# Optimization experiments

Measured on AMD Instinct MI355X. Metric: run time of the kernel, lower is better.

## Reference

```python
import jax, jax.numpy as jnp
import numpy as np

N = 2000
E = 128
H = 8
DH = E // H
K = 32  # max_neighbors
CLAMP = 1e4


def _sanitize(t):
    t = jnp.nan_to_num(t, nan=0.0, posinf=CLAMP, neginf=-CLAMP)
    return jnp.clip(t, -CLAMP, CLAMP)


def _layernorm(h, g, b, eps=1e-5):
    mu = h.mean(-1, keepdims=True)
    var = ((h - mu) ** 2).mean(-1, keepdims=True)
    return (h - mu) * jax.lax.rsqrt(var + eps) * g + b


def setup_inputs() -> dict:
    key = jax.random.key(0)
    ks = jax.random.split(key, 8)
    x = jax.random.normal(ks[0], (N, E), dtype=jnp.float32)
    coords9 = jax.random.normal(ks[1], (N, 9), dtype=jnp.float32)
    prompt_signal = jax.random.normal(ks[2], (E,), dtype=jnp.float32)
    pe_w = jax.random.normal(ks[3], (3, 32), dtype=jnp.float32) / np.sqrt(3.0)
    pe_b = jnp.zeros((32,), jnp.float32)
    pe_g = jnp.ones((32,), jnp.float32)
    pe_bt = jnp.zeros((32,), jnp.float32)
    in_w = jax.random.normal(ks[4], (3 * E, E), dtype=jnp.float32) / np.sqrt(E)
    in_b = jnp.zeros((3 * E,), jnp.float32)
    out_w = jax.random.normal(ks[5], (E, E), dtype=jnp.float32) / np.sqrt(E)
    out_b = jnp.zeros((E,), jnp.float32)
    return {"x": x, "coords9": coords9, "prompt_signal": prompt_signal,
            "pe_w": pe_w, "pe_b": pe_b, "pe_g": pe_g, "pe_bt": pe_bt,
            "in_w": in_w, "in_b": in_b, "out_w": out_w, "out_b": out_b}


def reference(x, coords9, prompt_signal, pe_w, pe_b, pe_g, pe_bt, in_w, in_b, out_w, out_b):
    n = x.shape[0]
    verts = coords9.reshape(n, 3, 3)
    cent = verts.mean(axis=1)  # (N,3)

    # pairwise centroid distances (only geo-relation channel that affects the output;
    # cos_angles/area_ratios/boundary_sharing feed geo_bias which is dead code in forward)
    diff = cent[:, None, :] - cent[None, :, :]
    dist = jnp.sqrt(jnp.sum(diff * diff, axis=-1) + 1e-20)  # (N,N)

    # positional encoder: Linear(3,32) -> GELU(exact) -> LayerNorm(32)
    pe = jax.nn.gelu(cent @ pe_w + pe_b, approximate=False)
    pe = _layernorm(pe, pe_g, pe_bt)  # (N,32)

    prompt_enhanced = x + prompt_signal[None, :]
    pos_enhanced = jnp.concatenate([prompt_enhanced[:, : 3 * E // 4], pe], axis=-1)  # (N,128)

    # top-K nearest neighbors -> additive attention mask (0 for kept, -inf-like otherwise)
    _, topk_idx = jax.lax.top_k(-dist, K)  # (N,K) smallest distances
    big_neg = jnp.float32(-1e9)
    attn_mask = jnp.full((n, n), big_neg, dtype=jnp.float32)
    attn_mask = attn_mask.at[jnp.arange(n)[:, None], topk_idx].set(0.0)

    # nn.MultiheadAttention (self-attention, eval mode -> no dropout)
    qkv = pos_enhanced @ in_w.T + in_b  # (N,3E)
    q, k, v = jnp.split(qkv, 3, axis=-1)
    q = q.reshape(n, H, DH).transpose(1, 0, 2)  # (H,N,DH)
    k = k.reshape(n, H, DH).transpose(1, 0, 2)
    v = v.reshape(n, H, DH).transpose(1, 0, 2)
    scores = jnp.einsum('hnd,hmd->hnm', q, k) / np.sqrt(DH) + attn_mask[None]
    probs = jax.nn.softmax(scores, axis=-1)
    o = jnp.einsum('hnm,hmd->hnd', probs, v)  # (H,N,DH)
    o = o.transpose(1, 0, 2).reshape(n, E)
    out = o @ out_w.T + out_b
    return _sanitize(out)
```

## Files before the change

kernel.cpp:

```cpp
#include <hip/hip_runtime.h>
#include <math.h>

#define N_NODES 2000
#define E_DIM   128
#define QKV_W   384
#define LDA     36
#define GEMM_BLOCKS 189

__global__ __launch_bounds__(256) void prep_qkv_kernel(
    const float* __restrict__ x, const float* __restrict__ coords9,
    const float* __restrict__ ps, const float* __restrict__ pe_w,
    const float* __restrict__ pe_b, const float* __restrict__ pe_g,
    const float* __restrict__ pe_bt, const float* __restrict__ in_w,
    const float* __restrict__ in_b, const float* __restrict__ out_w,
    float4* __restrict__ cw, float* __restrict__ qkv,
    float* __restrict__ out_wT)
{
    __shared__ __align__(16) float As[E_DIM * LDA];
    int tid = threadIdx.x;

    if (blockIdx.x >= GEMM_BLOCKS) {
        int bid2 = blockIdx.x - GEMM_BLOCKS;
        int g2 = tid >> 5, lane2 = tid & 31;
        int k = bid2 * 8 + g2;
        #pragma unroll
        for (int m = 0; m < 4; ++m) {
            int e = lane2 + 32 * m;
            out_wT[k * 128 + e] = out_w[e * 128 + k];
        }
        return;
    }

    int rt = blockIdx.x / 3, ct = blockIdx.x % 3;
    int rbase = rt * 32, cbase = ct * 128;
    int g = tid >> 5, lane = tid & 31;

    #pragma unroll
    for (int rr = 0; rr < 4; ++rr) {
        int rl = rr * 8 + g;
        int row = rbase + rl;
        bool vr = (row < N_NODES);
        float cx = 0.f, cy = 0.f, cz = 0.f;
        if (vr) {
            const float* c9 = coords9 + row * 9;
            cx = (c9[0] + c9[3] + c9[6]) * (1.0f / 3.0f);
            cy = (c9[1] + c9[4] + c9[7]) * (1.0f / 3.0f);
            cz = (c9[2] + c9[5] + c9[8]) * (1.0f / 3.0f);
        }
        if (ct == 0 && vr && lane == 0) {
            float4 c4; c4.x = cx; c4.y = cy; c4.z = cz; c4.w = 0.f;
            cw[row] = c4;
        }

        #pragma unroll
        for (int k = 0; k < 3; ++k) {
            int c = lane + 32 * k;
            float v = vr ? (x[row * E_DIM + c] + ps[c]) : 0.f;
            As[c * LDA + rl] = v;
        }

        int j = lane;
        float h = cx * pe_w[j] + cy * pe_w[32 + j] + cz * pe_w[64 + j] + pe_b[j];
        float ge = 0.5f * h * (1.0f + erff(h * 0.7071067811865476f));
        float s = ge;
        #pragma unroll
        for (int m = 16; m >= 1; m >>= 1) s += __shfl_xor(s, m);
        float mu = s * (1.0f / 32.0f);
        float d = ge - mu;
        float v2 = d * d;
        #pragma unroll
        for (int m = 16; m >= 1; m >>= 1) v2 += __shfl_xor(v2, m);
        float var = v2 * (1.0f / 32.0f);
        float y = d * (1.0f / sqrtf(var + 1e-5f)) * pe_g[j] + pe_bt[j];
        As[(96 + j) * LDA + rl] = vr ? y : 0.f;
    }
    __syncthreads();

    int cg = tid & 31, rg = tid >> 5;
    int c0 = cbase + cg * 4, r0 = rg * 4;
    float acc[4][4];
    #pragma unroll
    for (int i = 0; i < 4; ++i)
        #pragma unroll
        for (int jj = 0; jj < 4; ++jj) acc[i][jj] = 0.f;

    for (int k0 = 0; k0 < 128; k0 += 4) {
        float4 a0 = *(const float4*)&As[(k0 + 0) * LDA + r0];
        float4 a1 = *(const float4*)&As[(k0 + 1) * LDA + r0];
        float4 a2 = *(const float4*)&As[(k0 + 2) * LDA + r0];
        float4 a3 = *(const float4*)&As[(k0 + 3) * LDA + r0];
        #pragma unroll
        for (int ci = 0; ci < 4; ++ci) {
            float4 b = *(const float4*)&in_w[(c0 + ci) * E_DIM + k0];
            acc[0][ci] += a0.x * b.x + a1.x * b.y + a2.x * b.z + a3.x * b.w;
            acc[1][ci] += a0.y * b.x + a1.y * b.y + a2.y * b.z + a3.y * b.w;
            acc[2][ci] += a0.z * b.x + a1.z * b.y + a2.z * b.z + a3.z * b.w;
            acc[3][ci] += a0.w * b.x + a1.w * b.y + a2.w * b.z + a3.w * b.w;
        }
    }

    #pragma unroll
    for (int ri = 0; ri < 4; ++ri) {
        int row = rbase + r0 + ri;
        if (row < N_NODES) {
            float4 o4;
            o4.x = acc[ri][0] + in_b[c0 + 0];
            o4.y = acc[ri][1] + in_b[c0 + 1];
            o4.z = acc[ri][2] + in_b[c0 + 2];
            o4.w = acc[ri][3] + in_b[c0 + 3];
            *(float4*)&qkv[row * QKV_W + c0] = o4;
        }
    }
}

__device__ __forceinline__ float sanitize(float v)
{
    v = (v == v) ? v : 0.f;
    return fminf(fmaxf(v, -1e4f), 1e4f);
}

__global__ __launch_bounds__(256) void attn_proj_kernel(
    const float4* __restrict__ cw, const float* __restrict__ qkv,
    const float* __restrict__ out_wT, const float* __restrict__ out_b,
    float* __restrict__ out)
{
    __shared__ unsigned int hist[512];
    __shared__ float wMin[4], wMax[4];
    __shared__ int sh_b, sh_nless, sh_sel, sh_eq;
    __shared__ int waveSum[4];
    __shared__ int topk[32];
    __shared__ int eqIdx[256];
    __shared__ unsigned int eqKey[256];
    __shared__ __align__(16) float qs[128];
    __shared__ float pr[256];
    __shared__ __align__(16) float os[128];

    int tid = threadIdx.x;
    int row = blockIdx.x;
    int lane = tid & 63, wid = tid >> 6;

    float4 ci = cw[row];
    float cix = ci.x, ciy = ci.y, ciz = ci.z;
    unsigned int kbits[8];
    int bins[8];
    bool valid[8];
    float lmin = __int_as_float(0x7f800000);
    float lmax = __int_as_float(0xff800000);
    {
        #pragma clang fp contract(off)
        #pragma unroll
        for (int l = 0; l < 8; ++l) {
            int j = tid + 256 * l;
            valid[l] = (j < N_NODES);
            float key = __int_as_float(0x7f800000);
            if (valid[l]) {
                float4 cj = cw[j];
                float dx = cix - cj.x;
                float dy = ciy - cj.y;
                float dz = ciz - cj.z;
                float a = dx * dx;
                float b = dy * dy;
                float c = dz * dz;
                float d2 = ((a + b) + c) + 1e-20f;
                key = sqrtf(d2);
                lmin = fminf(lmin, key);
                lmax = fmaxf(lmax, key);
            }
            kbits[l] = __float_as_uint(key);
        }
    }

    #pragma unroll
    for (int m = 32; m >= 1; m >>= 1) {
        lmin = fminf(lmin, __shfl_xor(lmin, m));
        lmax = fmaxf(lmax, __shfl_xor(lmax, m));
    }
    if (lane == 0) { wMin[wid] = lmin; wMax[wid] = lmax; }
    hist[tid] = 0u;
    hist[tid + 256] = 0u;
    if (tid == 0) { sh_sel = 0; sh_eq = 0; }
    __syncthreads();
    float lo = fminf(fminf(wMin[0], wMin[1]), fminf(wMin[2], wMin[3]));
    float hi = fmaxf(fmaxf(wMax[0], wMax[1]), fmaxf(wMax[2], wMax[3]));
    float scale = 255.0f / fmaxf(hi - lo, 1e-30f);

    unsigned int hsel = (wid & 1) << 8;
    #pragma unroll
    for (int l = 0; l < 8; ++l) {
        int bin = 255;
        if (valid[l]) {
            float key = __uint_as_float(kbits[l]);
            bin = (int)((key - lo) * scale);
            bin = min(max(bin, 0), 255);
            atomicAdd(&hist[hsel + bin], 1u);
        }
        bins[l] = bin;
    }
    __syncthreads();

    int h = (int)(hist[tid] + hist[tid + 256]);
    int incl = h;
    #pragma unroll
    for (int dd = 1; dd < 64; dd <<= 1) {
        int u = __shfl_up(incl, dd);
        if (lane >= dd) incl += u;
    }
    if (lane == 63) waveSum[wid] = incl;
    __syncthreads();
    int off = 0;
    for (int w = 0; w < wid; ++w) off += waveSum[w];
    int cum = incl + off;
    if (cum >= 32 && (cum - h) < 32) {
        sh_b = tid;
        sh_nless = cum - h;
    }
    __syncthreads();

    int b = sh_b;
    int req = 32 - sh_nless;

    #pragma unroll
    for (int l = 0; l < 8; ++l) {
        if (valid[l]) {
            int bin = bins[l];
            int j = tid + 256 * l;
            if (bin < b) {
                int p = atomicAdd(&sh_sel, 1);
                topk[p] = j;
            } else if (bin == b) {
                int e = atomicAdd(&sh_eq, 1);
                if (e < 256) { eqIdx[e] = j; eqKey[e] = kbits[l]; }
            }
        }
    }
    if (tid < 128) qs[tid] = qkv[row * QKV_W + tid];
    __syncthreads();

    int eq = min(sh_eq, 256);
    if (tid < eq) {
        int myIdx = eqIdx[tid];
        unsigned int myKey = eqKey[tid];
        int rank = 0;
        for (int u = 0; u < eq; ++u) {
            unsigned int ku = eqKey[u];
            rank += (ku < myKey || (ku == myKey && eqIdx[u] < myIdx)) ? 1 : 0;
        }
        if (rank < req) {
            int p = atomicAdd(&sh_sel, 1);
            topk[p] = myIdx;
        }
    }
    __syncthreads();

    {
        int hh = tid >> 5, j = tid & 31;
        int jj = topk[j];
        const float4* kp = (const float4*)&qkv[jj * QKV_W + 128 + hh * 16];
        const float4* qp = (const float4*)&qs[hh * 16];
        float s = 0.f;
        #pragma unroll
        for (int i = 0; i < 4; ++i) {
            float4 kv = kp[i], qv = qp[i];
            s += qv.x * kv.x + qv.y * kv.y + qv.z * kv.z + qv.w * kv.w;
        }
        s *= 0.25f;
        float m = s;
        #pragma unroll
        for (int msk = 16; msk >= 1; msk >>= 1) m = fmaxf(m, __shfl_xor(m, msk));
        float p = expf(s - m);
        float su = p;
        #pragma unroll
        for (int msk = 16; msk >= 1; msk >>= 1) su += __shfl_xor(su, msk);
        pr[tid] = p / su;
    }
    __syncthreads();

    if (tid < 128) {
        int hh = tid >> 4;
        float acc = 0.f;
        #pragma unroll
        for (int j = 0; j < 32; ++j) {
            int jj = topk[j];
            acc += pr[hh * 32 + j] * qkv[jj * QKV_W + 256 + tid];
        }
        os[tid] = acc;
    }
    __syncthreads();

    if (tid < 128) {
        float a = 0.f;
        #pragma unroll
        for (int k = 0; k < 128; k += 4) {
            a += os[k + 0] * out_wT[(k + 0) * 128 + tid]
               + os[k + 1] * out_wT[(k + 1) * 128 + tid]
               + os[k + 2] * out_wT[(k + 2) * 128 + tid]
               + os[k + 3] * out_wT[(k + 3) * 128 + tid];
        }
        out[row * E_DIM + tid] = sanitize(a + out_b[tid]);
    }
}

extern "C" void kernel_launch(void* const* d_in, const int* in_sizes, int n_in,
                              void* d_out, int out_size, void* d_ws, size_t ws_size,
                              hipStream_t stream)
{
    const float* x      = (const float*)d_in[0];
    const float* coords = (const float*)d_in[1];
    const float* ps     = (const float*)d_in[2];
    const float* pe_w   = (const float*)d_in[3];
    const float* pe_b   = (const float*)d_in[4];
    const float* pe_g   = (const float*)d_in[5];
    const float* pe_bt  = (const float*)d_in[6];
    const float* in_w   = (const float*)d_in[7];
    const float* in_b   = (const float*)d_in[8];
    const float* out_w  = (const float*)d_in[9];
    const float* out_b  = (const float*)d_in[10];
    float* out = (float*)d_out;

    float* ws    = (float*)d_ws;
    float4* cw   = (float4*)ws;
    float* qkvb  = ws + 8192;
    float* owT   = ws + 8192 + 768000;

    prep_qkv_kernel<<<GEMM_BLOCKS + 16, 256, 0, stream>>>(
        x, coords, ps, pe_w, pe_b, pe_g, pe_bt, in_w, in_b, out_w,
        cw, qkvb, owT);
    attn_proj_kernel<<<2000, 256, 0, stream>>>(cw, qkvb, owT, out_b, out);
}
```

Measured before the change: 113.4 us.

## Process two query rows per block in attention kernel

Each block of the attention/projection kernel now handles two rows instead of one, launching half as many blocks. The candidate centroid loads are shared between both rows' distance computations, and the previously idle half of the threads now work in the value aggregation and output projection stages. This doubles shared memory and register use per block, which may reduce occupancy and serializes some per-row stages such as the tie-ranking and softmax.

```diff
diff --git a/kernel.cpp b/kernel.cpp
--- a/kernel.cpp
+++ b/kernel.cpp
@@ -124,143 +124,181 @@
     const float* __restrict__ out_wT, const float* __restrict__ out_b,
     float* __restrict__ out)
 {
-    __shared__ unsigned int hist[512];
-    __shared__ float wMin[4], wMax[4];
-    __shared__ int sh_b, sh_nless, sh_sel, sh_eq;
-    __shared__ int waveSum[4];
-    __shared__ int topk[32];
-    __shared__ int eqIdx[256];
-    __shared__ unsigned int eqKey[256];
-    __shared__ __align__(16) float qs[128];
-    __shared__ float pr[256];
-    __shared__ __align__(16) float os[128];
+    __shared__ unsigned int hist[1024];
+    __shared__ float wMinA[4], wMaxA[4], wMinB[4], wMaxB[4];
+    __shared__ int sh_b[2], sh_nless[2], sh_sel[2], sh_eq[2];
+    __shared__ int waveSumA[4], waveSumB[4];
+    __shared__ int topkA[32], topkB[32];
+    __shared__ int eqIdxA[256], eqIdxB[256];
+    __shared__ unsigned int eqKeyA[256], eqKeyB[256];
+    __shared__ __align__(16) float qsA[128], qsB[128];
+    __shared__ float prA[256], prB[256];
+    __shared__ __align__(16) float osA[128], osB[128];
 
     int tid = threadIdx.x;
-    int row = blockIdx.x;
+    int rA = blockIdx.x * 2, rB = rA + 1;
     int lane = tid & 63, wid = tid >> 6;
 
-    float4 ci = cw[row];
-    float cix = ci.x, ciy = ci.y, ciz = ci.z;
-    unsigned int kbits[8];
-    int bins[8];
+    float4 cAv = cw[rA], cBv = cw[rB];
+    unsigned int kbA[8], kbB[8];
+    int binsA[8], binsB[8];
     bool valid[8];
-    float lmin = __int_as_float(0x7f800000);
-    float lmax = __int_as_float(0xff800000);
+    float lminA = __int_as_float(0x7f800000), lmaxA = __int_as_float(0xff800000);
+    float lminB = __int_as_float(0x7f800000), lmaxB = __int_as_float(0xff800000);
     {
         #pragma clang fp contract(off)
         #pragma unroll
         for (int l = 0; l < 8; ++l) {
             int j = tid + 256 * l;
             valid[l] = (j < N_NODES);
-            float key = __int_as_float(0x7f800000);
+            float keyA = __int_as_float(0x7f800000);
+            float keyB = __int_as_float(0x7f800000);
             if (valid[l]) {
                 float4 cj = cw[j];
-                float dx = cix - cj.x;
-                float dy = ciy - cj.y;
-                float dz = ciz - cj.z;
-                float a = dx * dx;
-                float b = dy * dy;
-                float c = dz * dz;
-                float d2 = ((a + b) + c) + 1e-20f;
-                key = sqrtf(d2);
-                lmin = fminf(lmin, key);
-                lmax = fmaxf(lmax, key);
+                float dxA = cAv.x - cj.x, dyA = cAv.y - cj.y, dzA = cAv.z - cj.z;
+                float aA = dxA * dxA, bA = dyA * dyA, cA_ = dzA * dzA;
+                float d2A = ((aA + bA) + cA_) + 1e-20f;
+                keyA = sqrtf(d2A);
+                lminA = fminf(lminA, keyA);
+                lmaxA = fmaxf(lmaxA, keyA);
+                float dxB = cBv.x - cj.x, dyB = cBv.y - cj.y, dzB = cBv.z - cj.z;
+                float aB = dxB * dxB, bB = dyB * dyB, cB_ = dzB * dzB;
+                float d2B = ((aB + bB) + cB_) + 1e-20f;
+                keyB = sqrtf(d2B);
+                lminB = fminf(lminB, keyB);
+                lmaxB = fmaxf(lmaxB, keyB);
             }
-            kbits[l] = __float_as_uint(key);
+            kbA[l] = __float_as_uint(keyA);
+            kbB[l] = __float_as_uint(keyB);
         }
     }
 
     #pragma unroll
     for (int m = 32; m >= 1; m >>= 1) {
-        lmin = fminf(lmin, __shfl_xor(lmin, m));
-        lmax = fmaxf(lmax, __shfl_xor(lmax, m));
-    }
-    if (lane == 0) { wMin[wid] = lmin; wMax[wid] = lmax; }
-    hist[tid] = 0u;
-    hist[tid + 256] = 0u;
-    if (tid == 0) { sh_sel = 0; sh_eq = 0; }
-    __syncthreads();
-    float lo = fminf(fminf(wMin[0], wMin[1]), fminf(wMin[2], wMin[3]));
-    float hi = fmaxf(fmaxf(wMax[0], wMax[1]), fmaxf(wMax[2], wMax[3]));
-    float scale = 255.0f / fmaxf(hi - lo, 1e-30f);
-
-    unsigned int hsel = (wid & 1) << 8;
+        lminA = fminf(lminA, __shfl_xor(lminA, m));
+        lmaxA = fmaxf(lmaxA, __shfl_xor(lmaxA, m));
+        lminB = fminf(lminB, __shfl_xor(lminB, m));
+        lmaxB = fmaxf(lmaxB, __shfl_xor(lmaxB, m));
+    }
+    if (lane == 0) {
+        wMinA[wid] = lminA; wMaxA[wid] = lmaxA;
+        wMinB[wid] = lminB; wMaxB[wid] = lmaxB;
+    }
+    hist[tid] = 0u; hist[tid + 256] = 0u; hist[tid + 512] = 0u; hist[tid + 768] = 0u;
+    if (tid == 0) { sh_sel[0] = 0; sh_sel[1] = 0; sh_eq[0] = 0; sh_eq[1] = 0; }
+    __syncthreads();
+    float loA = fminf(fminf(wMinA[0], wMinA[1]), fminf(wMinA[2], wMinA[3]));
+    float hiA = fmaxf(fmaxf(wMaxA[0], wMaxA[1]), fmaxf(wMaxA[2], wMaxA[3]));
+    float scaleA = 255.0f / fmaxf(hiA - loA, 1e-30f);
+    float loB = fminf(fminf(wMinB[0], wMinB[1]), fminf(wMinB[2], wMinB[3]));
+    float hiB = fmaxf(fmaxf(wMaxB[0], wMaxB[1]), fmaxf(wMaxB[2], wMaxB[3]));
+    float scaleB = 255.0f / fmaxf(hiB - loB, 1e-30f);
+
+    unsigned int hselA = (unsigned int)(wid & 1) << 8;
+    unsigned int hselB = 512u + ((unsigned int)(wid & 1) << 8);
     #pragma unroll
     for (int l = 0; l < 8; ++l) {
-        int bin = 255;
+        int binA = 255, binB = 255;
         if (valid[l]) {
-            float key = __uint_as_float(kbits[l]);
-            bin = (int)((key - lo) * scale);
-            bin = min(max(bin, 0), 255);
-            atomicAdd(&hist[hsel + bin], 1u);
-        }
-        bins[l] = bin;
-    }
-    __syncthreads();
-
-    int h = (int)(hist[tid] + hist[tid + 256]);
-    int incl = h;
+            float keyA = __uint_as_float(kbA[l]);
+            binA = (int)((keyA - loA) * scaleA);
+            binA = min(max(binA, 0), 255);
+            atomicAdd(&hist[hselA + binA], 1u);
+            float keyB = __uint_as_float(kbB[l]);
+            binB = (int)((keyB - loB) * scaleB);
+            binB = min(max(binB, 0), 255);
+            atomicAdd(&hist[hselB + binB], 1u);
+        }
+        binsA[l] = binA; binsB[l] = binB;
+    }
+    __syncthreads();
+
+    int hA = (int)(hist[tid] + hist[tid + 256]);
+    int hB = (int)(hist[tid + 512] + hist[tid + 768]);
+    int inclA = hA, inclB = hB;
     #pragma unroll
     for (int dd = 1; dd < 64; dd <<= 1) {
-        int u = __shfl_up(incl, dd);
-        if (lane >= dd) incl += u;
-    }
-    if (lane == 63) waveSum[wid] = incl;
-    __syncthreads();
-    int off = 0;
-    for (int w = 0; w < wid; ++w) off += waveSum[w];
-    int cum = incl + off;
-    if (cum >= 32 && (cum - h) < 32) {
-        sh_b = tid;
-        sh_nless = cum - h;
-    }
-    __syncthreads();
-
-    int b = sh_b;
-    int req = 32 - sh_nless;
+        int uA = __shfl_up(inclA, dd);
+        int uB = __shfl_up(inclB, dd);
+        if (lane >= dd) { inclA += uA; inclB += uB; }
+    }
+    if (lane == 63) { waveSumA[wid] = inclA; waveSumB[wid] = inclB; }
+    __syncthreads();
+    int offA = 0, offB = 0;
+    for (int w = 0; w < wid; ++w) { offA += waveSumA[w]; offB += waveSumB[w]; }
+    int cumA = inclA + offA, cumB = inclB + offB;
+    if (cumA >= 32 && (cumA - hA) < 32) { sh_b[0] = tid; sh_nless[0] = cumA - hA; }
+    if (cumB >= 32 && (cumB - hB) < 32) { sh_b[1] = tid; sh_nless[1] = cumB - hB; }
+    __syncthreads();
+
+    int bA = sh_b[0], reqA = 32 - sh_nless[0];
+    int bB = sh_b[1], reqB = 32 - sh_nless[1];
 
     #pragma unroll
     for (int l = 0; l < 8; ++l) {
         if (valid[l]) {
-            int bin = bins[l];
             int j = tid + 256 * l;
-            if (bin < b) {
-                int p = atomicAdd(&sh_sel, 1);
-                topk[p] = j;
-            } else if (bin == b) {
-                int e = atomicAdd(&sh_eq, 1);
-                if (e < 256) { eqIdx[e] = j; eqKey[e] = kbits[l]; }
+            int binA = binsA[l];
+            if (binA < bA) {
+                int p = atomicAdd(&sh_sel[0], 1);
+                topkA[p] = j;
+            } else if (binA == bA) {
+                int e = atomicAdd(&sh_eq[0], 1);
+                if (e < 256) { eqIdxA[e] = j; eqKeyA[e] = kbA[l]; }
             }
-        }
-    }
-    if (tid < 128) qs[tid] = qkv[row * QKV_W + tid];
-    __syncthreads();
-
-    int eq = min(sh_eq, 256);
-    if (tid < eq) {
-        int myIdx = eqIdx[tid];
-        unsigned int myKey = eqKey[tid];
+            int binB = binsB[l];
+            if (binB < bB) {
+                int p = atomicAdd(&sh_sel[1], 1);
+                topkB[p] = j;
+            } else if (binB == bB) {
+                int e = atomicAdd(&sh_eq[1], 1);
+                if (e < 256) { eqIdxB[e] = j; eqKeyB[e] = kbB[l]; }
+            }
+        }
+    }
+    if (tid < 128) qsA[tid] = qkv[rA * QKV_W + tid];
+    else           qsB[tid - 128] = qkv[rB * QKV_W + (tid - 128)];
+    __syncthreads();
+
+    int eqA = min(sh_eq[0], 256);
+    if (tid < eqA) {
+        int myIdx = eqIdxA[tid];
+        unsigned int myKey = eqKeyA[tid];
         int rank = 0;
-        for (int u = 0; u < eq; ++u) {
-            unsigned int ku = eqKey[u];
-            rank += (ku < myKey || (ku == myKey && eqIdx[u] < myIdx)) ? 1 : 0;
-        }
-        if (rank < req) {
-            int p = atomicAdd(&sh_sel, 1);
-            topk[p] = myIdx;
+        for (int u = 0; u < eqA; ++u) {
+            unsigned int ku = eqKeyA[u];
+            rank += (ku < myKey || (ku == myKey && eqIdxA[u] < myIdx)) ? 1 : 0;
+        }
+        if (rank < reqA) {
+            int p = atomicAdd(&sh_sel[0], 1);
+            topkA[p] = myIdx;
+        }
+    }
+    int eqB = min(sh_eq[1], 256);
+    if (tid < eqB) {
+        int myIdx = eqIdxB[tid];
+        unsigned int myKey = eqKeyB[tid];
+        int rank = 0;
+        for (int u = 0; u < eqB; ++u) {
+            unsigned int ku = eqKeyB[u];
+            rank += (ku < myKey || (ku == myKey && eqIdxB[u] < myIdx)) ? 1 : 0;
+        }
+        if (rank < reqB) {
+            int p = atomicAdd(&sh_sel[1], 1);
+            topkB[p] = myIdx;
         }
     }
     __syncthreads();
 
     {
         int hh = tid >> 5, j = tid & 31;
-        int jj = topk[j];
-        const float4* kp = (const float4*)&qkv[jj * QKV_W + 128 + hh * 16];
-        const float4* qp = (const float4*)&qs[hh * 16];
+        const float4* qpA = (const float4*)&qsA[hh * 16];
+        int jjA = topkA[j];
+        const float4* kpA = (const float4*)&qkv[jjA * QKV_W + 128 + hh * 16];
         float s = 0.f;
         #pragma unroll
         for (int i = 0; i < 4; ++i) {
-            float4 kv = kp[i], qv = qp[i];
+            float4 kv = kpA[i], qv = qpA[i];
             s += qv.x * kv.x + qv.y * kv.y + qv.z * kv.z + qv.w * kv.w;
         }
         s *= 0.25f;
@@ -271,32 +309,65 @@
         float su = p;
         #pragma unroll
         for (int msk = 16; msk >= 1; msk >>= 1) su += __shfl_xor(su, msk);
-        pr[tid] = p / su;
-    }
-    __syncthreads();
-
-    if (tid < 128) {
-        int hh = tid >> 4;
-        float acc = 0.f;
-        #pragma unroll
-        for (int j = 0; j < 32; ++j) {
-            int jj = topk[j];
-            acc += pr[hh * 32 + j] * qkv[jj * QKV_W + 256 + tid];
-        }
-        os[tid] = acc;
-    }
-    __syncthreads();
-
-    if (tid < 128) {
+        prA[tid] = p / su;
+
+        const float4* qpB = (const float4*)&qsB[hh * 16];
+        int jjB = topkB[j];
+        const float4* kpB = (const float4*)&qkv[jjB * QKV_W + 128 + hh * 16];
+        float s2 = 0.f;
+        #pragma unroll
+        for (int i = 0; i < 4; ++i) {
+            float4 kv = kpB[i], qv = qpB[i];
+            s2 += qv.x * kv.x + qv.y * kv.y + qv.z * kv.z + qv.w * kv.w;
+        }
+        s2 *= 0.25f;
+        float m2 = s2;
+        #pragma unroll
+        for (int msk = 16; msk >= 1; msk >>= 1) m2 = fmaxf(m2, __shfl_xor(m2, msk));
+        float p2 = expf(s2 - m2);
+        float su2 = p2;
+        #pragma unroll
+        for (int msk = 16; msk >= 1; msk >>= 1) su2 += __shfl_xor(su2, msk);
+        prB[tid] = p2 / su2;
+    }
+    __syncthreads();
+
+    {
+        int e = tid & 127;
+        int hh = e >> 4;
+        if (tid < 128) {
+            float acc = 0.f;
+            #pragma unroll
+            for (int j = 0; j < 32; ++j) {
+                int jj = topkA[j];
+                acc += prA[hh * 32 + j] * qkv[jj * QKV_W + 256 + e];
+            }
+            osA[e] = acc;
+        } else {
+            float acc = 0.f;
+            #pragma unroll
+            for (int j = 0; j < 32; ++j) {
+                int jj = topkB[j];
+                acc += prB[hh * 32 + j] * qkv[jj * QKV_W + 256 + e];
+            }
+            osB[e] = acc;
+        }
+    }
+    __syncthreads();
+
+    {
+        int e = tid & 127;
+        const float* osp = (tid < 128) ? osA : osB;
+        int orow = (tid < 128) ? rA : rB;
         float a = 0.f;
         #pragma unroll
         for (int k = 0; k < 128; k += 4) {
-            a += os[k + 0] * out_wT[(k + 0) * 128 + tid]
-               + os[k + 1] * out_wT[(k + 1) * 128 + tid]
-               + os[k + 2] * out_wT[(k + 2) * 128 + tid]
-               + os[k + 3] * out_wT[(k + 3) * 128 + tid];
-        }
-        out[row * E_DIM + tid] = sanitize(a + out_b[tid]);
+            a += osp[k + 0] * out_wT[(k + 0) * 128 + e]
+               + osp[k + 1] * out_wT[(k + 1) * 128 + e]
+               + osp[k + 2] * out_wT[(k + 2) * 128 + e]
+               + osp[k + 3] * out_wT[(k + 3) * 128 + e];
+        }
+        out[orow * E_DIM + e] = sanitize(a + out_b[e]);
     }
 }
 
@@ -325,5 +396,5 @@
     prep_qkv_kernel<<<GEMM_BLOCKS + 16, 256, 0, stream>>>(
         x, coords, ps, pe_w, pe_b, pe_g, pe_bt, in_w, in_b, out_w,
         cw, qkvb, owT);
-    attn_proj_kernel<<<2000, 256, 0, stream>>>(cw, qkvb, owT, out_b, out);
+    attn_proj_kernel<<<N_NODES / 2, 256, 0, stream>>>(cw, qkvb, owT, out_b, out);
 }
```

Measured after the change: 114.2 us. Within noise of the previous version (+0.7%).
